# Optimization experiments

Measured on AMD Instinct MI355X. Metric: run time of the kernel, lower is better.

Reference implementation:

```python
import jax, jax.numpy as jnp
import numpy as np

N = 50000          # nodes
E = 800000         # edges
F_IN, H, OUT = 512, 256, 2
BN_EPS = 1e-5


def setup_inputs() -> dict:
    key = jax.random.key(0)
    ks = jax.random.split(key, 10)
    x = jax.random.normal(ks[0], (N, F_IN), jnp.float32)
    edge_index = jax.random.randint(ks[1], (2, E), 0, N, dtype=jnp.int64)
    edge_weight = jax.random.uniform(ks[2], (E,), jnp.float32)

    def lin(k, fan_in, fan_out):
        return jax.random.normal(k, (fan_in, fan_out), jnp.float32) / np.sqrt(fan_in).astype(np.float32)

    W1, b1 = lin(ks[3], F_IN, H), jnp.zeros((H,), jnp.float32)
    W2, b2 = lin(ks[4], H, H), jnp.zeros((H,), jnp.float32)
    W3, b3 = lin(ks[5], H, OUT), jnp.zeros((OUT,), jnp.float32)
    # BatchNorm1d affine params + running stats (eval mode)
    g1, be1 = jnp.ones((H,), jnp.float32), jnp.zeros((H,), jnp.float32)
    m1 = 0.1 * jax.random.normal(ks[6], (H,), jnp.float32)
    v1 = jax.random.uniform(ks[7], (H,), jnp.float32, 0.5, 1.5)
    g2, be2 = jnp.ones((H,), jnp.float32), jnp.zeros((H,), jnp.float32)
    m2 = 0.1 * jax.random.normal(ks[8], (H,), jnp.float32)
    v2 = jax.random.uniform(ks[9], (H,), jnp.float32, 0.5, 1.5)
    return {"x": x, "edge_index": edge_index, "edge_weight": edge_weight,
            "W1": W1, "b1": b1, "g1": g1, "be1": be1, "m1": m1, "v1": v1,
            "W2": W2, "b2": b2, "g2": g2, "be2": be2, "m2": m2, "v2": v2,
            "W3": W3, "b3": b3}


def gcn_conv(x, row, col, w, W, b):
    # PyG GCNConv (eval): h = x @ W; out[col] += norm * h[row]; + b
    # row/col/w already include self-loops with weight 1.
    n = x.shape[0]
    h = x @ W                                      # [N, out]
    deg = jax.ops.segment_sum(w, col, num_segments=n)
    dinv = jnp.where(deg > 0, jax.lax.rsqrt(deg), 0.0)
    norm = dinv[row] * w * dinv[col]               # [E+N]
    out = jax.ops.segment_sum(h[row] * norm[:, None], col, num_segments=n)
    return out + b


def batchnorm_eval(x, g, be, m, v):
    return (x - m) * jax.lax.rsqrt(v + BN_EPS) * g + be


def reference(x, edge_index, edge_weight, W1, b1, g1, be1, m1, v1,
              W2, b2, g2, be2, m2, v2, W3, b3):
    n = x.shape[0]
    loops = jnp.arange(n, dtype=edge_index.dtype)
    row = jnp.concatenate([edge_index[0], loops])
    col = jnp.concatenate([edge_index[1], loops])
    w = jnp.concatenate([edge_weight, jnp.ones((n,), x.dtype)])

    h = jax.nn.relu(batchnorm_eval(gcn_conv(x, row, col, w, W1, b1), g1, be1, m1, v1))
    h = jax.nn.relu(batchnorm_eval(gcn_conv(h, row, col, w, W2, b2), g2, be2, m2, v2))
    return gcn_conv(h, row, col, w, W3, b3)
```

## Files before the change

### kernel.cpp

```cpp
#include <hip/hip_runtime.h>
#include <stdint.h>

#define F_IN 512
#define HF 256
#define OUT_F 2
#define BN_EPS 1e-5f
#define SCAN_B 256
#define LDSTR 36

typedef __attribute__((ext_vector_type(8))) short bf16x8;
typedef __attribute__((ext_vector_type(4))) float f32x4;

__device__ inline float bf2f(unsigned short u) {
    union { float f; uint32_t i; } v; v.i = ((uint32_t)u) << 16; return v.f;
}
__device__ inline unsigned short f2bf(float f) {
    union { float f; uint32_t i; } v; v.f = f;
    uint32_t r = v.i + 0x7FFFu + ((v.i >> 16) & 1u);
    return (unsigned short)(r >> 16);
}

__global__ void prep_kernel(unsigned long long* __restrict__ packed,
                            const float* __restrict__ W1, unsigned short* __restrict__ W1t,
                            const float* __restrict__ W2, unsigned short* __restrict__ W2t,
                            int n) {
    int idx = blockIdx.x * blockDim.x + threadIdx.x;
    if (idx < n) { packed[idx] = 1ULL << 20; return; }
    int j = idx - n;
    if (j < F_IN * HF) {
        int nn = j >> 9, k = j & (F_IN - 1);
        W1t[j] = f2bf(W1[(size_t)k * HF + nn]);
        return;
    }
    j -= F_IN * HF;
    if (j < HF * HF) {
        int nn = j >> 8, k = j & (HF - 1);
        W2t[j] = f2bf(W2[(size_t)k * HF + nn]);
    }
}

template<int A_IS_F32>
__device__ __forceinline__
void gemm_body(const void* __restrict__ Araw, const unsigned short* __restrict__ Bt,
               unsigned short* __restrict__ C, int Mvalid, int K, int Ntot, int bid,
               unsigned short* As, unsigned short* Bs) {
    const int tid  = threadIdx.x;
    const int lane = tid & 63;
    const int wv   = tid >> 6;
    const int m0 = (bid >> 2) * 128;
    const int n0 = (bid & 3) * 64;

    const int sr = tid >> 2;
    const int sc = (tid & 3) * 8;

    f32x4 zero4 = {0.0f, 0.0f, 0.0f, 0.0f};
    f32x4 acc[2][4];
    #pragma unroll
    for (int i = 0; i < 2; ++i)
        #pragma unroll
        for (int j = 0; j < 4; ++j) acc[i][j] = zero4;

    const int q8 = (lane >> 4) * 8;
    const int ml = lane & 15;

    for (int k0 = 0; k0 < K; k0 += 32) {
        if (A_IS_F32) {
            const float* A = (const float*)Araw;
            #pragma unroll
            for (int h = 0; h < 2; ++h) {
                int rr = sr + h * 64;
                int gm = m0 + rr;
                float4 f0 = {0.f, 0.f, 0.f, 0.f}, f1 = {0.f, 0.f, 0.f, 0.f};
                if (gm < Mvalid) {
                    f0 = *(const float4*)(A + (size_t)gm * K + k0 + sc);
                    f1 = *(const float4*)(A + (size_t)gm * K + k0 + sc + 4);
                }
                bf16x8 v;
                v[0] = (short)f2bf(f0.x); v[1] = (short)f2bf(f0.y);
                v[2] = (short)f2bf(f0.z); v[3] = (short)f2bf(f0.w);
                v[4] = (short)f2bf(f1.x); v[5] = (short)f2bf(f1.y);
                v[6] = (short)f2bf(f1.z); v[7] = (short)f2bf(f1.w);
                *(bf16x8*)&As[rr * LDSTR + sc] = v;
            }
        } else {
            const unsigned short* A = (const unsigned short*)Araw;
            #pragma unroll
            for (int h = 0; h < 2; ++h) {
                int rr = sr + h * 64;
                int gm = m0 + rr;
                bf16x8 v = {0, 0, 0, 0, 0, 0, 0, 0};
                if (gm < Mvalid) v = *(const bf16x8*)(A + (size_t)gm * K + k0 + sc);
                *(bf16x8*)&As[rr * LDSTR + sc] = v;
            }
        }
        {
            bf16x8 v = *(const bf16x8*)(Bt + (size_t)(n0 + sr) * K + k0 + sc);
            *(bf16x8*)&Bs[sr * LDSTR + sc] = v;
        }
        __syncthreads();

        bf16x8 af[2], bfr[4];
        #pragma unroll
        for (int i = 0; i < 2; ++i)
            af[i] = *(const bf16x8*)&As[(wv * 32 + i * 16 + ml) * LDSTR + q8];
        #pragma unroll
        for (int j = 0; j < 4; ++j)
            bfr[j] = *(const bf16x8*)&Bs[(j * 16 + ml) * LDSTR + q8];
        #pragma unroll
        for (int i = 0; i < 2; ++i)
            #pragma unroll
            for (int j = 0; j < 4; ++j)
                acc[i][j] = __builtin_amdgcn_mfma_f32_16x16x32_bf16(af[i], bfr[j], acc[i][j], 0, 0, 0);
        __syncthreads();
    }

    const int q4 = (lane >> 4) * 4;
    #pragma unroll
    for (int i = 0; i < 2; ++i) {
        #pragma unroll
        for (int j = 0; j < 4; ++j) {
            #pragma unroll
            for (int rg = 0; rg < 4; ++rg) {
                int r = m0 + wv * 32 + i * 16 + q4 + rg;
                int c = n0 + j * 16 + ml;
                C[(size_t)r * Ntot + c] = f2bf(acc[i][j][rg]);
            }
        }
    }
}

__global__ __launch_bounds__(256)
void gemm1_count_kernel(const float* __restrict__ x, const unsigned short* __restrict__ W1t,
                        unsigned short* __restrict__ C,
                        const int* __restrict__ col, const float* __restrict__ w,
                        unsigned long long* __restrict__ packed,
                        int Mvalid, int e, int ngemm) {
    __shared__ unsigned short As[128 * LDSTR];
    __shared__ unsigned short Bs[64 * LDSTR];
    int bid = blockIdx.x;
    if (bid < ngemm) {
        gemm_body<1>(x, W1t, C, Mvalid, F_IN, HF, bid, As, Bs);
    } else {
        int base = (bid - ngemm) * 1024 + (int)threadIdx.x;
        #pragma unroll
        for (int k = 0; k < 4; ++k) {
            int i = base + k * 256;
            if (i < e) {
                unsigned long long add = (1ULL << 40)
                    | (unsigned long long)__float2uint_rn(w[i] * 1048576.0f);
                atomicAdd(&packed[col[i]], add);
            }
        }
    }
}

__global__ __launch_bounds__(256)
void gemm2_kernel(const unsigned short* __restrict__ A, const unsigned short* __restrict__ Bt,
                  unsigned short* __restrict__ C, int Mvalid) {
    __shared__ unsigned short As[128 * LDSTR];
    __shared__ unsigned short Bs[64 * LDSTR];
    gemm_body<0>(A, Bt, C, Mvalid, HF, HF, blockIdx.x, As, Bs);
}

__global__ void scan1_kernel(const unsigned long long* __restrict__ packed,
                             int* __restrict__ local, int* __restrict__ blocksum, int n) {
    __shared__ int tmp[SCAN_B];
    int i = blockIdx.x * SCAN_B + threadIdx.x;
    int v = (i < n) ? (int)(packed[i] >> 40) : 0;
    tmp[threadIdx.x] = v;
    __syncthreads();
    for (int off = 1; off < SCAN_B; off <<= 1) {
        int t = 0;
        if ((int)threadIdx.x >= off) t = tmp[threadIdx.x - off];
        __syncthreads();
        if ((int)threadIdx.x >= off) tmp[threadIdx.x] += t;
        __syncthreads();
    }
    if (i < n) local[i] = tmp[threadIdx.x] - v;
    if (threadIdx.x == SCAN_B - 1) blocksum[blockIdx.x] = tmp[SCAN_B - 1];
}

__global__ void scan3_dinv_kernel(int* __restrict__ csr_ptr, int* __restrict__ cursor,
                                  const int* __restrict__ blocksum,
                                  const unsigned long long* __restrict__ packed,
                                  float* __restrict__ dinv, int n, int e, int nb) {
    __shared__ int red[SCAN_B];
    int t = threadIdx.x;
    red[t] = (t < nb && t < (int)blockIdx.x) ? blocksum[t] : 0;
    __syncthreads();
    for (int off = SCAN_B / 2; off > 0; off >>= 1) {
        if (t < off) red[t] += red[t + off];
        __syncthreads();
    }
    int prefix = red[0];
    int i = blockIdx.x * SCAN_B + t;
    if (i < n) {
        int val = csr_ptr[i] + prefix;
        csr_ptr[i] = val;
        cursor[i] = val;
        float deg = (float)(packed[i] & 0xFFFFFFFFFFULL) * (1.0f / 1048576.0f);
        dinv[i] = rsqrtf(deg);
    }
    if (i == 0) csr_ptr[n] = e;
}

__global__ void fill_kernel(const int* __restrict__ row, const int* __restrict__ col,
                            const float* __restrict__ w, const float* __restrict__ dinv,
                            int* __restrict__ cursor, int2* __restrict__ csr_edge, int e) {
    int i = blockIdx.x * blockDim.x + threadIdx.x;
    if (i < e) {
        int r = row[i], c = col[i];
        int pos = atomicAdd(&cursor[c], 1);
        float nrm = dinv[r] * w[i] * dinv[c];
        csr_edge[pos] = make_int2(r, __float_as_int(nrm));
    }
}

template<int FINAL>
__global__ void agg_kernel(const unsigned short* __restrict__ h,
                           const int* __restrict__ ptr,
                           const int2* __restrict__ edge,
                           const float* __restrict__ dinv,
                           const float* __restrict__ b, const float* __restrict__ g,
                           const float* __restrict__ be, const float* __restrict__ m,
                           const float* __restrict__ v,
                           unsigned short* __restrict__ out,
                           const float* __restrict__ W3, float* __restrict__ h3, int n) {
    int wid  = (blockIdx.x * blockDim.x + threadIdx.x) >> 6;
    int lane = threadIdx.x & 63;
    if (wid >= n) return;
    int p0 = ptr[wid], p1 = ptr[wid + 1];
    const int fo = lane * 4;
    float a0 = 0.f, a1 = 0.f, a2 = 0.f, a3 = 0.f;

    const int pend = p0 + ((p1 - p0) & ~7);
    for (int p = p0; p < pend; p += 8) {
        int2 ed[8];
        #pragma unroll
        for (int k = 0; k < 8; ++k) ed[k] = edge[p + k];
        ushort4 hv[8];
        #pragma unroll
        for (int k = 0; k < 8; ++k)
            hv[k] = *(const ushort4*)(h + (size_t)ed[k].x * HF + fo);
        #pragma unroll
        for (int k = 0; k < 8; ++k) {
            float nw = __int_as_float(ed[k].y);
            a0 += nw * bf2f(hv[k].x);
            a1 += nw * bf2f(hv[k].y);
            a2 += nw * bf2f(hv[k].z);
            a3 += nw * bf2f(hv[k].w);
        }
    }
    if (pend < p1) {
        int2 ed[8];
        float wv[8];
        #pragma unroll
        for (int k = 0; k < 8; ++k) {
            int idx = pend + k < p1 ? pend + k : p1 - 1;
            ed[k] = edge[idx];
            wv[k] = (pend + k < p1) ? __int_as_float(ed[k].y) : 0.0f;
        }
        ushort4 hv[8];
        #pragma unroll
        for (int k = 0; k < 8; ++k)
            hv[k] = *(const ushort4*)(h + (size_t)ed[k].x * HF + fo);
        #pragma unroll
        for (int k = 0; k < 8; ++k) {
            a0 += wv[k] * bf2f(hv[k].x);
            a1 += wv[k] * bf2f(hv[k].y);
            a2 += wv[k] * bf2f(hv[k].z);
            a3 += wv[k] * bf2f(hv[k].w);
        }
    }
    float s = dinv[wid];
    float sl = s * s;
    ushort4 hv = *(const ushort4*)(h + (size_t)wid * HF + fo);
    a0 += sl * bf2f(hv.x);
    a1 += sl * bf2f(hv.y);
    a2 += sl * bf2f(hv.z);
    a3 += sl * bf2f(hv.w);

    float4 bb  = *(const float4*)(b + fo);
    float4 gg  = *(const float4*)(g + fo);
    float4 bee = *(const float4*)(be + fo);
    float4 mm  = *(const float4*)(m + fo);
    float4 vv  = *(const float4*)(v + fo);
    float f0 = fmaxf((a0 + bb.x - mm.x) * rsqrtf(vv.x + BN_EPS) * gg.x + bee.x, 0.f);
    float f1 = fmaxf((a1 + bb.y - mm.y) * rsqrtf(vv.y + BN_EPS) * gg.y + bee.y, 0.f);
    float f2 = fmaxf((a2 + bb.z - mm.z) * rsqrtf(vv.z + BN_EPS) * gg.z + bee.z, 0.f);
    float f3 = fmaxf((a3 + bb.w - mm.w) * rsqrtf(vv.w + BN_EPS) * gg.w + bee.w, 0.f);

    if (!FINAL) {
        ushort4 o;
        o.x = f2bf(f0); o.y = f2bf(f1); o.z = f2bf(f2); o.w = f2bf(f3);
        *(ushort4*)(out + (size_t)wid * HF + fo) = o;
    } else {
        float4 w0 = *(const float4*)(W3 + fo * 2);
        float4 w1 = *(const float4*)(W3 + fo * 2 + 4);
        float s0 = f0 * w0.x + f1 * w0.z + f2 * w1.x + f3 * w1.z;
        float s1 = f0 * w0.y + f1 * w0.w + f2 * w1.y + f3 * w1.w;
        #pragma unroll
        for (int o = 32; o > 0; o >>= 1) {
            s0 += __shfl_down(s0, o, 64);
            s1 += __shfl_down(s1, o, 64);
        }
        if (lane == 0) {
            h3[wid * 2 + 0] = s0;
            h3[wid * 2 + 1] = s1;
        }
    }
}

__global__ void out_kernel(const float* __restrict__ h3,
                           const int* __restrict__ ptr, const int2* __restrict__ edge,
                           const float* __restrict__ dinv,
                           const float* __restrict__ b3, float* __restrict__ out, int n) {
    int i = blockIdx.x * blockDim.x + threadIdx.x;
    if (i >= n) return;
    int p0 = ptr[i], p1 = ptr[i + 1];
    float a0 = 0.f, a1 = 0.f;
    for (int p = p0; p < p1; p += 4) {
        #pragma unroll
        for (int k = 0; k < 4; ++k) {
            int idx = p + k < p1 ? p + k : p1 - 1;
            int2 e = edge[idx];
            float nw = (p + k < p1) ? __int_as_float(e.y) : 0.0f;
            float2 u = *(const float2*)(h3 + 2 * e.x);
            a0 += nw * u.x;
            a1 += nw * u.y;
        }
    }
    float s = dinv[i];
    float sl = s * s;
    out[2 * i + 0] = a0 + sl * h3[2 * i + 0] + b3[0];
    out[2 * i + 1] = a1 + sl * h3[2 * i + 1] + b3[1];
}

static inline char* align16(char* p) {
    return (char*)(((uintptr_t)p + 15) & ~(uintptr_t)15);
}

extern "C" void kernel_launch(void* const* d_in, const int* in_sizes, int n_in,
                              void* d_out, int out_size, void* d_ws, size_t ws_size,
                              hipStream_t stream) {
    const float* x   = (const float*)d_in[0];
    const int*   ei  = (const int*)d_in[1];
    const float* ew  = (const float*)d_in[2];
    const float* W1  = (const float*)d_in[3];
    const float* b1  = (const float*)d_in[4];
    const float* g1  = (const float*)d_in[5];
    const float* be1 = (const float*)d_in[6];
    const float* m1  = (const float*)d_in[7];
    const float* v1  = (const float*)d_in[8];
    const float* W2  = (const float*)d_in[9];
    const float* b2  = (const float*)d_in[10];
    const float* g2  = (const float*)d_in[11];
    const float* be2 = (const float*)d_in[12];
    const float* m2  = (const float*)d_in[13];
    const float* v2  = (const float*)d_in[14];
    const float* W3  = (const float*)d_in[15];
    const float* b3  = (const float*)d_in[16];

    const int N  = in_sizes[0] / F_IN;
    const int E  = in_sizes[2];
    const int MP = (N + 127) & ~127;
    const int* row = ei;
    const int* col = ei + E;

    char* wsb = (char*)d_ws;
    unsigned long long* packed = (unsigned long long*)wsb; wsb = align16(wsb + (size_t)N * 8);
    float* dinv     = (float*)wsb;          wsb = align16(wsb + (size_t)N * 4);
    int*   csr_ptr  = (int*)wsb;            wsb = align16(wsb + (size_t)(N + 1) * 4);
    int*   cursor   = (int*)wsb;            wsb = align16(wsb + (size_t)N * 4);
    int*   blocksum = (int*)wsb;            wsb = align16(wsb + (size_t)SCAN_B * 4);
    int2*  csr_edge = (int2*)wsb;           wsb = align16(wsb + (size_t)E * 8);
    unsigned short* W1t = (unsigned short*)wsb;  wsb = align16(wsb + (size_t)F_IN * HF * 2);
    unsigned short* W2t = (unsigned short*)wsb;  wsb = align16(wsb + (size_t)HF * HF * 2);
    unsigned short* bufh = (unsigned short*)wsb; wsb = align16(wsb + (size_t)MP * HF * 2);
    unsigned short* bufa = (unsigned short*)wsb; wsb = align16(wsb + (size_t)MP * HF * 2);
    float* h3 = (float*)wsb;                wsb = align16(wsb + (size_t)N * OUT_F * 4);
    float* outf = (float*)d_out;

    const int TB = 256;
    const int nscan = (N + SCAN_B - 1) / SCAN_B;
    const int preptot = N + F_IN * HF + HF * HF;
    const int ngemm = (MP / 128) * 4;
    const int ncount = (E + 1023) / 1024;

    prep_kernel<<<(preptot + TB - 1) / TB, TB, 0, stream>>>(packed, W1, W1t, W2, W2t, N);

    gemm1_count_kernel<<<ngemm + ncount, TB, 0, stream>>>(
        x, W1t, bufh, col, ew, packed, N, E, ngemm);

    scan1_kernel<<<nscan, SCAN_B, 0, stream>>>(packed, csr_ptr, blocksum, N);
    scan3_dinv_kernel<<<nscan, SCAN_B, 0, stream>>>(csr_ptr, cursor, blocksum, packed, dinv, N, E, nscan);
    fill_kernel<<<(E + TB - 1) / TB, TB, 0, stream>>>(row, col, ew, dinv, cursor, csr_edge, E);

    agg_kernel<0><<<((size_t)N * 64 + TB - 1) / TB, TB, 0, stream>>>(
        bufh, csr_ptr, csr_edge, dinv, b1, g1, be1, m1, v1, bufa, nullptr, nullptr, N);

    gemm2_kernel<<<ngemm, TB, 0, stream>>>(bufa, W2t, bufh, MP);

    agg_kernel<1><<<((size_t)N * 64 + TB - 1) / TB, TB, 0, stream>>>(
        bufh, csr_ptr, csr_edge, dinv, b2, g2, be2, m2, v2, nullptr, W3, h3, N);

    out_kernel<<<(N + TB - 1) / TB, TB, 0, stream>>>(h3, csr_ptr, csr_edge, dinv, b3, outf, N);
}
```

Before: 528.7 us.

## Retile GEMMs to 64xfull-N blocks so A is read once per row

The GEMM tiling changes from 128x64 output tiles (4 column blocks per row strip) to 64x256 tiles covering the full output width. Each block now stages all 256 B rows per K step, and each wave issues 16 MFMAs with a single A fragment. This avoids re-reading and re-converting the fp32 x input four times across column blocks, which matters most for the 512-wide first layer. The count-block section is also moved to the front of the fused launch so the atomic-heavy degree counting starts first. In exchange each block holds more LDS (B tile) and 16 accumulators, which may lower occupancy, and more blocks reload B from cache.

Result: slower. 638.0 us (+20.7%).

```diff
diff --git a/kernel.cpp b/kernel.cpp
--- a/kernel.cpp
+++ b/kernel.cpp
@@ -42,23 +42,20 @@
 template<int A_IS_F32>
 __device__ __forceinline__
 void gemm_body(const void* __restrict__ Araw, const unsigned short* __restrict__ Bt,
-               unsigned short* __restrict__ C, int Mvalid, int K, int Ntot, int bid,
+               unsigned short* __restrict__ C, int Mvalid, int K, int mblk,
                unsigned short* As, unsigned short* Bs) {
     const int tid  = threadIdx.x;
     const int lane = tid & 63;
     const int wv   = tid >> 6;
-    const int m0 = (bid >> 2) * 128;
-    const int n0 = (bid & 3) * 64;
+    const int m0 = mblk * 64;
 
     const int sr = tid >> 2;
     const int sc = (tid & 3) * 8;
 
     f32x4 zero4 = {0.0f, 0.0f, 0.0f, 0.0f};
-    f32x4 acc[2][4];
+    f32x4 acc[16];
     #pragma unroll
-    for (int i = 0; i < 2; ++i)
-        #pragma unroll
-        for (int j = 0; j < 4; ++j) acc[i][j] = zero4;
+    for (int j = 0; j < 16; ++j) acc[j] = zero4;
 
     const int q8 = (lane >> 4) * 8;
     const int ml = lane & 15;
@@ -66,65 +63,50 @@
     for (int k0 = 0; k0 < K; k0 += 32) {
         if (A_IS_F32) {
             const float* A = (const float*)Araw;
-            #pragma unroll
-            for (int h = 0; h < 2; ++h) {
-                int rr = sr + h * 64;
-                int gm = m0 + rr;
-                float4 f0 = {0.f, 0.f, 0.f, 0.f}, f1 = {0.f, 0.f, 0.f, 0.f};
-                if (gm < Mvalid) {
-                    f0 = *(const float4*)(A + (size_t)gm * K + k0 + sc);
-                    f1 = *(const float4*)(A + (size_t)gm * K + k0 + sc + 4);
-                }
-                bf16x8 v;
-                v[0] = (short)f2bf(f0.x); v[1] = (short)f2bf(f0.y);
-                v[2] = (short)f2bf(f0.z); v[3] = (short)f2bf(f0.w);
-                v[4] = (short)f2bf(f1.x); v[5] = (short)f2bf(f1.y);
-                v[6] = (short)f2bf(f1.z); v[7] = (short)f2bf(f1.w);
-                *(bf16x8*)&As[rr * LDSTR + sc] = v;
+            int gm = m0 + sr;
+            float4 f0 = {0.f, 0.f, 0.f, 0.f}, f1 = {0.f, 0.f, 0.f, 0.f};
+            if (gm < Mvalid) {
+                f0 = *(const float4*)(A + (size_t)gm * K + k0 + sc);
+                f1 = *(const float4*)(A + (size_t)gm * K + k0 + sc + 4);
             }
+            bf16x8 v;
+            v[0] = (short)f2bf(f0.x); v[1] = (short)f2bf(f0.y);
+            v[2] = (short)f2bf(f0.z); v[3] = (short)f2bf(f0.w);
+            v[4] = (short)f2bf(f1.x); v[5] = (short)f2bf(f1.y);
+            v[6] = (short)f2bf(f1.z); v[7] = (short)f2bf(f1.w);
+            *(bf16x8*)&As[sr * LDSTR + sc] = v;
         } else {
             const unsigned short* A = (const unsigned short*)Araw;
-            #pragma unroll
-            for (int h = 0; h < 2; ++h) {
-                int rr = sr + h * 64;
-                int gm = m0 + rr;
-                bf16x8 v = {0, 0, 0, 0, 0, 0, 0, 0};
-                if (gm < Mvalid) v = *(const bf16x8*)(A + (size_t)gm * K + k0 + sc);
-                *(bf16x8*)&As[rr * LDSTR + sc] = v;
-            }
-        }
-        {
-            bf16x8 v = *(const bf16x8*)(Bt + (size_t)(n0 + sr) * K + k0 + sc);
-            *(bf16x8*)&Bs[sr * LDSTR + sc] = v;
-        }
-        __syncthreads();
-
-        bf16x8 af[2], bfr[4];
-        #pragma unroll
-        for (int i = 0; i < 2; ++i)
-            af[i] = *(const bf16x8*)&As[(wv * 32 + i * 16 + ml) * LDSTR + q8];
-        #pragma unroll
-        for (int j = 0; j < 4; ++j)
-            bfr[j] = *(const bf16x8*)&Bs[(j * 16 + ml) * LDSTR + q8];
-        #pragma unroll
-        for (int i = 0; i < 2; ++i)
-            #pragma unroll
-            for (int j = 0; j < 4; ++j)
-                acc[i][j] = __builtin_amdgcn_mfma_f32_16x16x32_bf16(af[i], bfr[j], acc[i][j], 0, 0, 0);
+            int gm = m0 + sr;
+            bf16x8 v = {0, 0, 0, 0, 0, 0, 0, 0};
+            if (gm < Mvalid) v = *(const bf16x8*)(A + (size_t)gm * K + k0 + sc);
+            *(bf16x8*)&As[sr * LDSTR + sc] = v;
+        }
+        #pragma unroll
+        for (int h = 0; h < 4; ++h) {
+            int rr = sr + h * 64;
+            bf16x8 v = *(const bf16x8*)(Bt + (size_t)rr * K + k0 + sc);
+            *(bf16x8*)&Bs[rr * LDSTR + sc] = v;
+        }
+        __syncthreads();
+
+        bf16x8 af = *(const bf16x8*)&As[(wv * 16 + ml) * LDSTR + q8];
+        #pragma unroll
+        for (int j = 0; j < 16; ++j) {
+            bf16x8 bfr = *(const bf16x8*)&Bs[(j * 16 + ml) * LDSTR + q8];
+            acc[j] = __builtin_amdgcn_mfma_f32_16x16x32_bf16(af, bfr, acc[j], 0, 0, 0);
+        }
         __syncthreads();
     }
 
     const int q4 = (lane >> 4) * 4;
     #pragma unroll
-    for (int i = 0; i < 2; ++i) {
-        #pragma unroll
-        for (int j = 0; j < 4; ++j) {
-            #pragma unroll
-            for (int rg = 0; rg < 4; ++rg) {
-                int r = m0 + wv * 32 + i * 16 + q4 + rg;
-                int c = n0 + j * 16 + ml;
-                C[(size_t)r * Ntot + c] = f2bf(acc[i][j][rg]);
-            }
+    for (int j = 0; j < 16; ++j) {
+        #pragma unroll
+        for (int rg = 0; rg < 4; ++rg) {
+            int r = m0 + wv * 16 + q4 + rg;
+            int c = j * 16 + ml;
+            C[(size_t)r * HF + c] = f2bf(acc[j][rg]);
         }
     }
 }
@@ -134,14 +116,12 @@
                         unsigned short* __restrict__ C,
                         const int* __restrict__ col, const float* __restrict__ w,
                         unsigned long long* __restrict__ packed,
-                        int Mvalid, int e, int ngemm) {
-    __shared__ unsigned short As[128 * LDSTR];
-    __shared__ unsigned short Bs[64 * LDSTR];
+                        int Mvalid, int e, int ncount) {
+    __shared__ unsigned short As[64 * LDSTR];
+    __shared__ unsigned short Bs[256 * LDSTR];
     int bid = blockIdx.x;
-    if (bid < ngemm) {
-        gemm_body<1>(x, W1t, C, Mvalid, F_IN, HF, bid, As, Bs);
-    } else {
-        int base = (bid - ngemm) * 1024 + (int)threadIdx.x;
+    if (bid < ncount) {
+        int base = bid * 1024 + (int)threadIdx.x;
         #pragma unroll
         for (int k = 0; k < 4; ++k) {
             int i = base + k * 256;
@@ -151,15 +131,17 @@
                 atomicAdd(&packed[col[i]], add);
             }
         }
+    } else {
+        gemm_body<1>(x, W1t, C, Mvalid, F_IN, bid - ncount, As, Bs);
     }
 }
 
 __global__ __launch_bounds__(256)
 void gemm2_kernel(const unsigned short* __restrict__ A, const unsigned short* __restrict__ Bt,
                   unsigned short* __restrict__ C, int Mvalid) {
-    __shared__ unsigned short As[128 * LDSTR];
-    __shared__ unsigned short Bs[64 * LDSTR];
-    gemm_body<0>(A, Bt, C, Mvalid, HF, HF, blockIdx.x, As, Bs);
+    __shared__ unsigned short As[64 * LDSTR];
+    __shared__ unsigned short Bs[256 * LDSTR];
+    gemm_body<0>(A, Bt, C, Mvalid, HF, blockIdx.x, As, Bs);
 }
 
 __global__ void scan1_kernel(const unsigned long long* __restrict__ packed,
@@ -363,7 +345,7 @@
 
     const int N  = in_sizes[0] / F_IN;
     const int E  = in_sizes[2];
-    const int MP = (N + 127) & ~127;
+    const int MP = (N + 63) & ~63;
     const int* row = ei;
     const int* col = ei + E;
 
@@ -384,13 +366,13 @@
     const int TB = 256;
     const int nscan = (N + SCAN_B - 1) / SCAN_B;
     const int preptot = N + F_IN * HF + HF * HF;
-    const int ngemm = (MP / 128) * 4;
+    const int ngemm = MP / 64;
     const int ncount = (E + 1023) / 1024;
 
     prep_kernel<<<(preptot + TB - 1) / TB, TB, 0, stream>>>(packed, W1, W1t, W2, W2t, N);
 
-    gemm1_count_kernel<<<ngemm + ncount, TB, 0, stream>>>(
-        x, W1t, bufh, col, ew, packed, N, E, ngemm);
+    gemm1_count_kernel<<<ncount + ngemm, TB, 0, stream>>>(
+        x, W1t, bufh, col, ew, packed, N, E, ncount);
 
     scan1_kernel<<<nscan, SCAN_B, 0, stream>>>(packed, csr_ptr, blocksum, N);
     scan3_dinv_kernel<<<nscan, SCAN_B, 0, stream>>>(csr_ptr, cursor, blocksum, packed, dinv, N, E, nscan);
```

## Enlarge GEMM tiles to 128x128 with LDS-staged coalesced epilogue, split count kernel

Applied to the files above, without the earlier changes.

The GEMM block tile grows from 128x64 to 128x128, arranged as a 2x2 wave grid with a 64x64 sub-tile per wave. The A-tile is now reused across twice as many output columns, which halves the number of times x is reloaded and converted from fp32. The epilogue stages bf16 results through LDS so each row is written with 16-byte coalesced stores instead of scattered 2-byte writes. The edge-count atomics move out of the fused gemm1 kernel into their own kernel, and gemm1 now launches after the CSR build. This gives up the earlier overlap between the GEMM and the atomic counting, and the larger accumulator raises register use.

New measurement: 534.9 us. Within noise of the previous version (+1.2%).

```diff
diff --git a/kernel.cpp b/kernel.cpp
--- a/kernel.cpp
+++ b/kernel.cpp
@@ -7,6 +7,7 @@
 #define BN_EPS 1e-5f
 #define SCAN_B 256
 #define LDSTR 36
+#define EPSTR 136
 
 typedef __attribute__((ext_vector_type(8))) short bf16x8;
 typedef __attribute__((ext_vector_type(4))) float f32x4;
@@ -39,29 +40,44 @@
     }
 }
 
+__global__ void count_pack_kernel(const int* __restrict__ col,
+                                  const float* __restrict__ w,
+                                  unsigned long long* __restrict__ packed, int e) {
+    int i = blockIdx.x * blockDim.x + threadIdx.x;
+    if (i < e) {
+        unsigned long long add = (1ULL << 40)
+            | (unsigned long long)__float2uint_rn(w[i] * 1048576.0f);
+        atomicAdd(&packed[col[i]], add);
+    }
+}
+
 template<int A_IS_F32>
 __device__ __forceinline__
 void gemm_body(const void* __restrict__ Araw, const unsigned short* __restrict__ Bt,
-               unsigned short* __restrict__ C, int Mvalid, int K, int Ntot, int bid,
-               unsigned short* As, unsigned short* Bs) {
+               unsigned short* __restrict__ C, int Mvalid, int K, int Ntot,
+               int mblk, int nblk, char* smem) {
+    unsigned short* As = (unsigned short*)smem;
+    unsigned short* Bs = As + 128 * LDSTR;
     const int tid  = threadIdx.x;
     const int lane = tid & 63;
     const int wv   = tid >> 6;
-    const int m0 = (bid >> 2) * 128;
-    const int n0 = (bid & 3) * 64;
+    const int wrow = wv >> 1, wcol = wv & 1;
+    const int m0 = mblk * 128;
+    const int n0 = nblk * 128;
 
     const int sr = tid >> 2;
     const int sc = (tid & 3) * 8;
 
     f32x4 zero4 = {0.0f, 0.0f, 0.0f, 0.0f};
-    f32x4 acc[2][4];
+    f32x4 acc[4][4];
     #pragma unroll
-    for (int i = 0; i < 2; ++i)
+    for (int i = 0; i < 4; ++i)
         #pragma unroll
         for (int j = 0; j < 4; ++j) acc[i][j] = zero4;
 
     const int q8 = (lane >> 4) * 8;
     const int ml = lane & 15;
+    const int q4 = (lane >> 4) * 4;
 
     for (int k0 = 0; k0 < K; k0 += 32) {
         if (A_IS_F32) {
@@ -93,73 +109,71 @@
                 *(bf16x8*)&As[rr * LDSTR + sc] = v;
             }
         }
-        {
-            bf16x8 v = *(const bf16x8*)(Bt + (size_t)(n0 + sr) * K + k0 + sc);
-            *(bf16x8*)&Bs[sr * LDSTR + sc] = v;
-        }
-        __syncthreads();
-
-        bf16x8 af[2], bfr[4];
-        #pragma unroll
-        for (int i = 0; i < 2; ++i)
-            af[i] = *(const bf16x8*)&As[(wv * 32 + i * 16 + ml) * LDSTR + q8];
+        #pragma unroll
+        for (int h = 0; h < 2; ++h) {
+            int rr = sr + h * 64;
+            bf16x8 v = *(const bf16x8*)(Bt + (size_t)(nblk * 128 + rr) * K + k0 + sc);
+            *(bf16x8*)&Bs[rr * LDSTR + sc] = v;
+        }
+        __syncthreads();
+
+        bf16x8 af[4], bfr[4];
+        #pragma unroll
+        for (int i = 0; i < 4; ++i)
+            af[i] = *(const bf16x8*)&As[(wrow * 64 + i * 16 + ml) * LDSTR + q8];
         #pragma unroll
         for (int j = 0; j < 4; ++j)
-            bfr[j] = *(const bf16x8*)&Bs[(j * 16 + ml) * LDSTR + q8];
-        #pragma unroll
-        for (int i = 0; i < 2; ++i)
+            bfr[j] = *(const bf16x8*)&Bs[(wcol * 64 + j * 16 + ml) * LDSTR + q8];
+        #pragma unroll
+        for (int i = 0; i < 4; ++i)
             #pragma unroll
             for (int j = 0; j < 4; ++j)
-                acc[i][j] = __builtin_amdgcn_mfma_f32_16x16x32_bf16(af[i], bfr[j], acc[i][j], 0, 0, 0);
-        __syncthreads();
-    }
-
-    const int q4 = (lane >> 4) * 4;
+                acc[i][j] = __builtin_amdgcn_mfma_f32_16x16x32_bf16(bfr[j], af[i], acc[i][j], 0, 0, 0);
+        __syncthreads();
+    }
+
+    unsigned short* Ep = (unsigned short*)smem;
     #pragma unroll
-    for (int i = 0; i < 2; ++i) {
-        #pragma unroll
-        for (int j = 0; j < 4; ++j) {
+    for (int hh = 0; hh < 2; ++hh) {
+        if (wrow == hh) {
             #pragma unroll
-            for (int rg = 0; rg < 4; ++rg) {
-                int r = m0 + wv * 32 + i * 16 + q4 + rg;
-                int c = n0 + j * 16 + ml;
-                C[(size_t)r * Ntot + c] = f2bf(acc[i][j][rg]);
+            for (int i = 0; i < 4; ++i) {
+                #pragma unroll
+                for (int j = 0; j < 4; ++j) {
+                    short4 o;
+                    o.x = (short)f2bf(acc[i][j][0]);
+                    o.y = (short)f2bf(acc[i][j][1]);
+                    o.z = (short)f2bf(acc[i][j][2]);
+                    o.w = (short)f2bf(acc[i][j][3]);
+                    *(short4*)&Ep[(i * 16 + ml) * EPSTR + wcol * 64 + j * 16 + q4] = o;
+                }
             }
         }
+        __syncthreads();
+        #pragma unroll
+        for (int rnd = 0; rnd < 4; ++rnd) {
+            int rowh = (tid >> 4) + rnd * 16;
+            int ch   = tid & 15;
+            bf16x8 v = *(const bf16x8*)&Ep[rowh * EPSTR + ch * 8];
+            int gr = m0 + hh * 64 + rowh;
+            *(bf16x8*)(C + (size_t)gr * Ntot + n0 + ch * 8) = v;
+        }
+        __syncthreads();
     }
 }
 
 __global__ __launch_bounds__(256)
-void gemm1_count_kernel(const float* __restrict__ x, const unsigned short* __restrict__ W1t,
-                        unsigned short* __restrict__ C,
-                        const int* __restrict__ col, const float* __restrict__ w,
-                        unsigned long long* __restrict__ packed,
-                        int Mvalid, int e, int ngemm) {
-    __shared__ unsigned short As[128 * LDSTR];
-    __shared__ unsigned short Bs[64 * LDSTR];
-    int bid = blockIdx.x;
-    if (bid < ngemm) {
-        gemm_body<1>(x, W1t, C, Mvalid, F_IN, HF, bid, As, Bs);
-    } else {
-        int base = (bid - ngemm) * 1024 + (int)threadIdx.x;
-        #pragma unroll
-        for (int k = 0; k < 4; ++k) {
-            int i = base + k * 256;
-            if (i < e) {
-                unsigned long long add = (1ULL << 40)
-                    | (unsigned long long)__float2uint_rn(w[i] * 1048576.0f);
-                atomicAdd(&packed[col[i]], add);
-            }
-        }
-    }
+void gemm1_kernel(const float* __restrict__ x, const unsigned short* __restrict__ W1t,
+                  unsigned short* __restrict__ C, int Mvalid) {
+    __shared__ __align__(16) char smem[2 * 128 * LDSTR * 2];
+    gemm_body<1>(x, W1t, C, Mvalid, F_IN, HF, blockIdx.x, blockIdx.y, smem);
 }
 
 __global__ __launch_bounds__(256)
 void gemm2_kernel(const unsigned short* __restrict__ A, const unsigned short* __restrict__ Bt,
                   unsigned short* __restrict__ C, int Mvalid) {
-    __shared__ unsigned short As[128 * LDSTR];
-    __shared__ unsigned short Bs[64 * LDSTR];
-    gemm_body<0>(A, Bt, C, Mvalid, HF, HF, blockIdx.x, As, Bs);
+    __shared__ __align__(16) char smem[2 * 128 * LDSTR * 2];
+    gemm_body<0>(A, Bt, C, Mvalid, HF, HF, blockIdx.x, blockIdx.y, smem);
 }
 
 __global__ void scan1_kernel(const unsigned long long* __restrict__ packed,
@@ -384,23 +398,21 @@
     const int TB = 256;
     const int nscan = (N + SCAN_B - 1) / SCAN_B;
     const int preptot = N + F_IN * HF + HF * HF;
-    const int ngemm = (MP / 128) * 4;
-    const int ncount = (E + 1023) / 1024;
 
     prep_kernel<<<(preptot + TB - 1) / TB, TB, 0, stream>>>(packed, W1, W1t, W2, W2t, N);
 
-    gemm1_count_kernel<<<ngemm + ncount, TB, 0, stream>>>(
-        x, W1t, bufh, col, ew, packed, N, E, ngemm);
-
+    count_pack_kernel<<<(E + TB - 1) / TB, TB, 0, stream>>>(col, ew, packed, E);
     scan1_kernel<<<nscan, SCAN_B, 0, stream>>>(packed, csr_ptr, blocksum, N);
     scan3_dinv_kernel<<<nscan, SCAN_B, 0, stream>>>(csr_ptr, cursor, blocksum, packed, dinv, N, E, nscan);
     fill_kernel<<<(E + TB - 1) / TB, TB, 0, stream>>>(row, col, ew, dinv, cursor, csr_edge, E);
 
+    dim3 ggrid(MP / 128, HF / 128);
+
+    gemm1_kernel<<<ggrid, TB, 0, stream>>>(x, W1t, bufh, N);
     agg_kernel<0><<<((size_t)N * 64 + TB - 1) / TB, TB, 0, stream>>>(
         bufh, csr_ptr, csr_edge, dinv, b1, g1, be1, m1, v1, bufa, nullptr, nullptr, N);
 
-    gemm2_kernel<<<ngemm, TB, 0, stream>>>(bufa, W2t, bufh, MP);
-
+    gemm2_kernel<<<ggrid, TB, 0, stream>>>(bufa, W2t, bufh, N);
     agg_kernel<1><<<((size_t)N * 64 + TB - 1) / TB, TB, 0, stream>>>(
         bufh, csr_ptr, csr_edge, dinv, b2, g2, be2, m2, v2, nullptr, W3, h3, N);
 
```

## Pre-convert x to bf16 and use double-buffered 128x128 GEMM tiles

Applied to the files above, without the earlier changes.

Moves the fp32-to-bf16 conversion of x out of the GEMM into the edge-count kernel, which writes a padded bf16 copy. Pad rows are zeroed in the prep kernel so the GEMM can drop its bounds checks. The GEMM is replaced by a unified kernel with 128x128 tiles, a 2x2 warp layout, register prefetch and double-buffered LDS, using one sync per k-step. This cuts GEMM launches and improves data reuse, but adds a full extra pass over x (read fp32, write bf16) and the GEMM no longer overlaps with the atomic counting.

New measurement: 492.5 us. 6.8% less time.

```diff
diff --git a/kernel.cpp b/kernel.cpp
--- a/kernel.cpp
+++ b/kernel.cpp
@@ -23,7 +23,9 @@
 __global__ void prep_kernel(unsigned long long* __restrict__ packed,
                             const float* __restrict__ W1, unsigned short* __restrict__ W1t,
                             const float* __restrict__ W2, unsigned short* __restrict__ W2t,
-                            int n) {
+                            unsigned short* __restrict__ xbf_pad,
+                            unsigned short* __restrict__ bufa_pad,
+                            int n, int padx, int pada) {
     int idx = blockIdx.x * blockDim.x + threadIdx.x;
     if (idx < n) { packed[idx] = 1ULL << 20; return; }
     int j = idx - n;
@@ -36,130 +38,123 @@
     if (j < HF * HF) {
         int nn = j >> 8, k = j & (HF - 1);
         W2t[j] = f2bf(W2[(size_t)k * HF + nn]);
-    }
-}
-
-template<int A_IS_F32>
-__device__ __forceinline__
-void gemm_body(const void* __restrict__ Araw, const unsigned short* __restrict__ Bt,
-               unsigned short* __restrict__ C, int Mvalid, int K, int Ntot, int bid,
-               unsigned short* As, unsigned short* Bs) {
+        return;
+    }
+    j -= HF * HF;
+    if (j < padx) { xbf_pad[j] = 0; return; }
+    j -= padx;
+    if (j < pada) bufa_pad[j] = 0;
+}
+
+__global__ void count_conv_kernel(const int* __restrict__ col,
+                                  const float* __restrict__ w,
+                                  unsigned long long* __restrict__ packed,
+                                  const float* __restrict__ x,
+                                  unsigned short* __restrict__ xbf,
+                                  int e, int nchunk) {
+    int tid = blockIdx.x * blockDim.x + threadIdx.x;
+    int base = blockIdx.x * 1024 + (int)threadIdx.x;
+    #pragma unroll
+    for (int k = 0; k < 4; ++k) {
+        int i = base + k * 256;
+        if (i < e) {
+            unsigned long long add = (1ULL << 40)
+                | (unsigned long long)__float2uint_rn(w[i] * 1048576.0f);
+            atomicAdd(&packed[col[i]], add);
+        }
+    }
+    const int stride = gridDim.x * blockDim.x;
+    const float4* x4 = (const float4*)x;
+    for (int c = tid; c < nchunk; c += stride) {
+        float4 f0 = x4[2 * c];
+        float4 f1 = x4[2 * c + 1];
+        bf16x8 v;
+        v[0] = (short)f2bf(f0.x); v[1] = (short)f2bf(f0.y);
+        v[2] = (short)f2bf(f0.z); v[3] = (short)f2bf(f0.w);
+        v[4] = (short)f2bf(f1.x); v[5] = (short)f2bf(f1.y);
+        v[6] = (short)f2bf(f1.z); v[7] = (short)f2bf(f1.w);
+        *(bf16x8*)(xbf + (size_t)c * 8) = v;
+    }
+}
+
+__global__ __launch_bounds__(256)
+void gemm_kernel(const unsigned short* __restrict__ A,
+                 const unsigned short* __restrict__ Bt,
+                 unsigned short* __restrict__ C, int K) {
+    __shared__ unsigned short As[2][128 * LDSTR];
+    __shared__ unsigned short Bs[2][128 * LDSTR];
     const int tid  = threadIdx.x;
     const int lane = tid & 63;
     const int wv   = tid >> 6;
-    const int m0 = (bid >> 2) * 128;
-    const int n0 = (bid & 3) * 64;
+    const int wrow = wv >> 1, wcol = wv & 1;
+    const int m0 = blockIdx.x * 128;
+    const int n0 = blockIdx.y * 128;
 
     const int sr = tid >> 2;
     const int sc = (tid & 3) * 8;
 
+    const unsigned short* pa0 = A + (size_t)(m0 + sr) * K + sc;
+    const unsigned short* pa1 = A + (size_t)(m0 + sr + 64) * K + sc;
+    const unsigned short* pb0 = Bt + (size_t)(n0 + sr) * K + sc;
+    const unsigned short* pb1 = Bt + (size_t)(n0 + sr + 64) * K + sc;
+
     f32x4 zero4 = {0.0f, 0.0f, 0.0f, 0.0f};
-    f32x4 acc[2][4];
+    f32x4 acc[4][4];
     #pragma unroll
-    for (int i = 0; i < 2; ++i)
+    for (int i = 0; i < 4; ++i)
         #pragma unroll
         for (int j = 0; j < 4; ++j) acc[i][j] = zero4;
 
     const int q8 = (lane >> 4) * 8;
     const int ml = lane & 15;
 
-    for (int k0 = 0; k0 < K; k0 += 32) {
-        if (A_IS_F32) {
-            const float* A = (const float*)Araw;
-            #pragma unroll
-            for (int h = 0; h < 2; ++h) {
-                int rr = sr + h * 64;
-                int gm = m0 + rr;
-                float4 f0 = {0.f, 0.f, 0.f, 0.f}, f1 = {0.f, 0.f, 0.f, 0.f};
-                if (gm < Mvalid) {
-                    f0 = *(const float4*)(A + (size_t)gm * K + k0 + sc);
-                    f1 = *(const float4*)(A + (size_t)gm * K + k0 + sc + 4);
-                }
-                bf16x8 v;
-                v[0] = (short)f2bf(f0.x); v[1] = (short)f2bf(f0.y);
-                v[2] = (short)f2bf(f0.z); v[3] = (short)f2bf(f0.w);
-                v[4] = (short)f2bf(f1.x); v[5] = (short)f2bf(f1.y);
-                v[6] = (short)f2bf(f1.z); v[7] = (short)f2bf(f1.w);
-                *(bf16x8*)&As[rr * LDSTR + sc] = v;
-            }
-        } else {
-            const unsigned short* A = (const unsigned short*)Araw;
-            #pragma unroll
-            for (int h = 0; h < 2; ++h) {
-                int rr = sr + h * 64;
-                int gm = m0 + rr;
-                bf16x8 v = {0, 0, 0, 0, 0, 0, 0, 0};
-                if (gm < Mvalid) v = *(const bf16x8*)(A + (size_t)gm * K + k0 + sc);
-                *(bf16x8*)&As[rr * LDSTR + sc] = v;
-            }
-        }
-        {
-            bf16x8 v = *(const bf16x8*)(Bt + (size_t)(n0 + sr) * K + k0 + sc);
-            *(bf16x8*)&Bs[sr * LDSTR + sc] = v;
-        }
+    bf16x8 va0 = *(const bf16x8*)pa0;
+    bf16x8 va1 = *(const bf16x8*)pa1;
+    bf16x8 vb0 = *(const bf16x8*)pb0;
+    bf16x8 vb1 = *(const bf16x8*)pb1;
+
+    const int nsteps = K >> 5;
+    for (int s = 0; s < nsteps; ++s) {
+        const int buf = s & 1;
+        *(bf16x8*)&As[buf][sr * LDSTR + sc]        = va0;
+        *(bf16x8*)&As[buf][(sr + 64) * LDSTR + sc] = va1;
+        *(bf16x8*)&Bs[buf][sr * LDSTR + sc]        = vb0;
+        *(bf16x8*)&Bs[buf][(sr + 64) * LDSTR + sc] = vb1;
         __syncthreads();
-
-        bf16x8 af[2], bfr[4];
-        #pragma unroll
-        for (int i = 0; i < 2; ++i)
-            af[i] = *(const bf16x8*)&As[(wv * 32 + i * 16 + ml) * LDSTR + q8];
+        if (s + 1 < nsteps) {
+            int off = (s + 1) * 32;
+            va0 = *(const bf16x8*)(pa0 + off);
+            va1 = *(const bf16x8*)(pa1 + off);
+            vb0 = *(const bf16x8*)(pb0 + off);
+            vb1 = *(const bf16x8*)(pb1 + off);
+        }
+        bf16x8 af[4], bfr[4];
+        #pragma unroll
+        for (int i = 0; i < 4; ++i)
+            af[i] = *(const bf16x8*)&As[buf][(wrow * 64 + i * 16 + ml) * LDSTR + q8];
         #pragma unroll
         for (int j = 0; j < 4; ++j)
-            bfr[j] = *(const bf16x8*)&Bs[(j * 16 + ml) * LDSTR + q8];
-        #pragma unroll
-        for (int i = 0; i < 2; ++i)
+            bfr[j] = *(const bf16x8*)&Bs[buf][(wcol * 64 + j * 16 + ml) * LDSTR + q8];
+        #pragma unroll
+        for (int i = 0; i < 4; ++i)
             #pragma unroll
             for (int j = 0; j < 4; ++j)
                 acc[i][j] = __builtin_amdgcn_mfma_f32_16x16x32_bf16(af[i], bfr[j], acc[i][j], 0, 0, 0);
-        __syncthreads();
     }
 
     const int q4 = (lane >> 4) * 4;
     #pragma unroll
-    for (int i = 0; i < 2; ++i) {
+    for (int i = 0; i < 4; ++i) {
         #pragma unroll
         for (int j = 0; j < 4; ++j) {
             #pragma unroll
             for (int rg = 0; rg < 4; ++rg) {
-                int r = m0 + wv * 32 + i * 16 + q4 + rg;
-                int c = n0 + j * 16 + ml;
-                C[(size_t)r * Ntot + c] = f2bf(acc[i][j][rg]);
+                int r = m0 + wrow * 64 + i * 16 + q4 + rg;
+                int c = n0 + wcol * 64 + j * 16 + ml;
+                C[(size_t)r * HF + c] = f2bf(acc[i][j][rg]);
             }
         }
     }
-}
-
-__global__ __launch_bounds__(256)
-void gemm1_count_kernel(const float* __restrict__ x, const unsigned short* __restrict__ W1t,
-                        unsigned short* __restrict__ C,
-                        const int* __restrict__ col, const float* __restrict__ w,
-                        unsigned long long* __restrict__ packed,
-                        int Mvalid, int e, int ngemm) {
-    __shared__ unsigned short As[128 * LDSTR];
-    __shared__ unsigned short Bs[64 * LDSTR];
-    int bid = blockIdx.x;
-    if (bid < ngemm) {
-        gemm_body<1>(x, W1t, C, Mvalid, F_IN, HF, bid, As, Bs);
-    } else {
-        int base = (bid - ngemm) * 1024 + (int)threadIdx.x;
-        #pragma unroll
-        for (int k = 0; k < 4; ++k) {
-            int i = base + k * 256;
-            if (i < e) {
-                unsigned long long add = (1ULL << 40)
-                    | (unsigned long long)__float2uint_rn(w[i] * 1048576.0f);
-                atomicAdd(&packed[col[i]], add);
-            }
-        }
-    }
-}
-
-__global__ __launch_bounds__(256)
-void gemm2_kernel(const unsigned short* __restrict__ A, const unsigned short* __restrict__ Bt,
-                  unsigned short* __restrict__ C, int Mvalid) {
-    __shared__ unsigned short As[128 * LDSTR];
-    __shared__ unsigned short Bs[64 * LDSTR];
-    gemm_body<0>(A, Bt, C, Mvalid, HF, HF, blockIdx.x, As, Bs);
 }
 
 __global__ void scan1_kernel(const unsigned long long* __restrict__ packed,
@@ -376,6 +371,7 @@
     int2*  csr_edge = (int2*)wsb;           wsb = align16(wsb + (size_t)E * 8);
     unsigned short* W1t = (unsigned short*)wsb;  wsb = align16(wsb + (size_t)F_IN * HF * 2);
     unsigned short* W2t = (unsigned short*)wsb;  wsb = align16(wsb + (size_t)HF * HF * 2);
+    unsigned short* xbf  = (unsigned short*)wsb; wsb = align16(wsb + (size_t)MP * F_IN * 2);
     unsigned short* bufh = (unsigned short*)wsb; wsb = align16(wsb + (size_t)MP * HF * 2);
     unsigned short* bufa = (unsigned short*)wsb; wsb = align16(wsb + (size_t)MP * HF * 2);
     float* h3 = (float*)wsb;                wsb = align16(wsb + (size_t)N * OUT_F * 4);
@@ -383,24 +379,28 @@
 
     const int TB = 256;
     const int nscan = (N + SCAN_B - 1) / SCAN_B;
-    const int preptot = N + F_IN * HF + HF * HF;
-    const int ngemm = (MP / 128) * 4;
+    const int padx = (MP - N) * F_IN;
+    const int pada = (MP - N) * HF;
+    const int preptot = N + F_IN * HF + HF * HF + padx + pada;
     const int ncount = (E + 1023) / 1024;
-
-    prep_kernel<<<(preptot + TB - 1) / TB, TB, 0, stream>>>(packed, W1, W1t, W2, W2t, N);
-
-    gemm1_count_kernel<<<ngemm + ncount, TB, 0, stream>>>(
-        x, W1t, bufh, col, ew, packed, N, E, ngemm);
+    const int nchunk = (N * F_IN) / 8;
+
+    prep_kernel<<<(preptot + TB - 1) / TB, TB, 0, stream>>>(
+        packed, W1, W1t, W2, W2t, xbf + (size_t)N * F_IN, bufa + (size_t)N * HF, N, padx, pada);
+
+    count_conv_kernel<<<ncount, TB, 0, stream>>>(col, ew, packed, x, xbf, E, nchunk);
 
     scan1_kernel<<<nscan, SCAN_B, 0, stream>>>(packed, csr_ptr, blocksum, N);
     scan3_dinv_kernel<<<nscan, SCAN_B, 0, stream>>>(csr_ptr, cursor, blocksum, packed, dinv, N, E, nscan);
     fill_kernel<<<(E + TB - 1) / TB, TB, 0, stream>>>(row, col, ew, dinv, cursor, csr_edge, E);
 
+    dim3 ggrid(MP / 128, HF / 128);
+
+    gemm_kernel<<<ggrid, TB, 0, stream>>>(xbf, W1t, bufh, F_IN);
     agg_kernel<0><<<((size_t)N * 64 + TB - 1) / TB, TB, 0, stream>>>(
         bufh, csr_ptr, csr_edge, dinv, b1, g1, be1, m1, v1, bufa, nullptr, nullptr, N);
 
-    gemm2_kernel<<<ngemm, TB, 0, stream>>>(bufa, W2t, bufh, MP);
-
+    gemm_kernel<<<ggrid, TB, 0, stream>>>(bufa, W2t, bufh, HF);
     agg_kernel<1><<<((size_t)N * 64 + TB - 1) / TB, TB, 0, stream>>>(
         bufh, csr_ptr, csr_edge, dinv, b2, g2, be2, m2, v2, nullptr, W3, h3, N);
 
```
